# Performance work log

Hardware: AMD Instinct MI355X
Metric: run time of the kernel (lower is better)

## Reference

```python
import jax, jax.numpy as jnp
import numpy as np
import math

B, L, C_IN = 32, 1024, 21
D_MODEL, N_HEADS, D_FF, E_LAYERS = 256, 8, 1024, 3
E = D_MODEL // N_HEADS
MOVING_AVG, FACTOR, NUM_CLASS = 5, 1.0, 3


def setup_inputs() -> dict:
    key = jax.random.key(0)
    ks = jax.random.split(key, 12)
    s = 0.05
    return {
        "x_enc": jax.random.normal(ks[0], (B, L, C_IN), jnp.float32),
        "token_w": jax.random.normal(ks[1], (D_MODEL, C_IN, 3), jnp.float32) * s,
        "qw": jax.random.normal(ks[2], (E_LAYERS, D_MODEL, D_MODEL), jnp.float32) * s,
        "qb": jnp.zeros((E_LAYERS, D_MODEL), jnp.float32),
        "kw": jax.random.normal(ks[3], (E_LAYERS, D_MODEL, D_MODEL), jnp.float32) * s,
        "kb": jnp.zeros((E_LAYERS, D_MODEL), jnp.float32),
        "vw": jax.random.normal(ks[4], (E_LAYERS, D_MODEL, D_MODEL), jnp.float32) * s,
        "vb": jnp.zeros((E_LAYERS, D_MODEL), jnp.float32),
        "ow": jax.random.normal(ks[5], (E_LAYERS, D_MODEL, D_MODEL), jnp.float32) * s,
        "ob": jnp.zeros((E_LAYERS, D_MODEL), jnp.float32),
        "c1w": jax.random.normal(ks[6], (E_LAYERS, D_FF, D_MODEL), jnp.float32) * s,
        "c2w": jax.random.normal(ks[7], (E_LAYERS, D_MODEL, D_FF), jnp.float32) * s,
        "norm_w": jnp.ones((D_MODEL,), jnp.float32),
        "norm_b": jnp.zeros((D_MODEL,), jnp.float32),
        "proj_w": jax.random.normal(ks[8], (NUM_CLASS, D_MODEL * L), jnp.float32) * 0.01,
        "proj_b": jnp.zeros((NUM_CLASS,), jnp.float32),
    }


def moving_mean(x, k):
    # x: (B, L, D); replicate-pad front/end by (k-1)//2 then average (AvgPool1d stride 1)
    p = (k - 1) // 2
    xp = jnp.concatenate([jnp.repeat(x[:, :1], p, 1), x, jnp.repeat(x[:, -1:], p, 1)], axis=1)
    Lx = x.shape[1]
    acc = xp[:, :Lx]
    for i in range(1, k):
        acc = acc + xp[:, i:i + Lx]
    return acc / k


def series_decomp(x, k):
    m = moving_mean(x, k)
    return x - m, m


def autocorrelation(q, k_, v):
    # q,k_,v: (B, L, H, E). Period-based dependency via FFT cross-correlation.
    Lq = q.shape[1]
    qf = jnp.fft.rfft(q.transpose(0, 2, 3, 1), axis=-1)   # (B,H,E,L//2+1)
    kf = jnp.fft.rfft(k_.transpose(0, 2, 3, 1), axis=-1)
    corr = jnp.fft.irfft(qf * jnp.conj(kf), n=Lq, axis=-1)  # (B,H,E,L)
    vals = v.transpose(0, 2, 3, 1)                          # (B,H,E,L)
    top_k = int(FACTOR * math.log(Lq))
    mean_corr = corr.mean(axis=(1, 2))                      # (B,L)
    weights, delay = jax.lax.top_k(mean_corr, top_k)        # (B,k)
    w = jax.nn.softmax(weights, axis=-1)                    # (B,k)
    # rolled gather: pattern[b,h,e,i,l] = vals[b,h,e,(l+delay[b,i]) % L]
    idx = (jnp.arange(Lq)[None, None, :] + delay[:, :, None]) % Lq  # (B,k,L)
    patterns = jax.vmap(lambda vb, ib: vb[:, :, ib])(vals, idx)      # (B,H,E,k,L)
    out = jnp.einsum('bhekl,bk->bhel', patterns, w)
    return out.transpose(0, 3, 1, 2)  # (B,L,H,E)


def encoder_layer(x, qw, qb, kw, kb, vw, vb, ow, ob, c1w, c2w):
    Bx, Lx, _ = x.shape
    q = (x @ qw.T + qb).reshape(Bx, Lx, N_HEADS, E)
    k_ = (x @ kw.T + kb).reshape(Bx, Lx, N_HEADS, E)
    v = (x @ vw.T + vb).reshape(Bx, Lx, N_HEADS, E)
    a = autocorrelation(q, k_, v).reshape(Bx, Lx, D_MODEL)
    a = a @ ow.T + ob
    x, _ = series_decomp(x + a, MOVING_AVG)
    y = jax.nn.gelu(jnp.einsum('bld,fd->blf', x, c1w), approximate=False)  # Conv1d k=1
    y = jnp.einsum('blf,df->bld', y, c2w)
    res, _ = series_decomp(x + y, MOVING_AVG)
    return res


def my_layernorm(x, w, b):
    mu = x.mean(-1, keepdims=True)
    var = ((x - mu) ** 2).mean(-1, keepdims=True)
    xh = (x - mu) / jnp.sqrt(var + 1e-5) * w + b
    return xh - xh.mean(axis=1, keepdims=True)  # subtract seasonal bias over time


def token_embed(x, w):
    # circular-padded Conv1d(C_IN -> D_MODEL, kernel 3, no bias)
    xt = x.transpose(0, 2, 1)                                   # (B,C,L)
    xp = jnp.pad(xt, ((0, 0), (0, 0), (1, 1)), mode='wrap')
    out = jax.lax.conv_general_dilated(xp, w, (1,), 'VALID')     # (B,D,L)
    return out.transpose(0, 2, 1)


def reference(x_enc, token_w, qw, qb, kw, kb, vw, vb, ow, ob, c1w, c2w, norm_w, norm_b, proj_w, proj_b):
    x = token_embed(x_enc, token_w)
    for l in range(E_LAYERS):
        x = encoder_layer(x, qw[l], qb[l], kw[l], kb[l], vw[l], vb[l], ow[l], ob[l], c1w[l], c2w[l])
    x = my_layernorm(x, norm_w, norm_b)
    out = jax.nn.gelu(x, approximate=False)
    out = out.reshape(out.shape[0], -1)  # (B, L*D_MODEL)
    return out @ proj_w.T + proj_b
```

## Files before the change

kernel.cpp:

```cpp
#include <hip/hip_runtime.h>
#include <hip/hip_bf16.h>
#include <math.h>

#define BB 32
#define LL 1024
#define C_IN 21
#define DM 256
#define DFF 1024
#define NLAYERS 3
#define TOPK 6
#define TOPC 16
#define LSCALE 4096.0f
#define LINV (1.0f/4096.0f)

typedef __attribute__((ext_vector_type(8))) short short8v;
typedef __attribute__((ext_vector_type(8))) _Float16 half8;
typedef __attribute__((ext_vector_type(4))) float f32x4;

__device__ __forceinline__ float gelu_f(float v){
    return 0.5f * v * (1.0f + erff(v * 0.7071067811865476f));
}
__device__ __forceinline__ ushort f2h_bits(float f){
    _Float16 h = (_Float16)f;
    return __builtin_bit_cast(ushort, h);
}
__device__ __forceinline__ float h2f(ushort u){
    return (float)__builtin_bit_cast(_Float16, u);
}
__device__ __forceinline__ void lds16(const ushort* g, ushort* l){
    __builtin_amdgcn_global_load_lds(
        (const __attribute__((address_space(1))) void*)g,
        (__attribute__((address_space(3))) void*)l, 16, 0, 0);
}
__device__ __forceinline__ float4 loadp4(const ushort* __restrict__ h, const ushort* __restrict__ l, size_t i4){
    ushort4 hv = *reinterpret_cast<const ushort4*>(h + 4*i4);
    ushort4 lv = *reinterpret_cast<const ushort4*>(l + 4*i4);
    return make_float4(h2f(hv.x)+h2f(lv.x)*LINV, h2f(hv.y)+h2f(lv.y)*LINV,
                       h2f(hv.z)+h2f(lv.z)*LINV, h2f(hv.w)+h2f(lv.w)*LINV);
}
__device__ __forceinline__ void storep4(ushort* __restrict__ h, ushort* __restrict__ l, size_t i4, float4 v){
    ushort4 hv, lv;
    _Float16 a;
    a=(_Float16)v.x; hv.x=__builtin_bit_cast(ushort,a); lv.x=f2h_bits((v.x-(float)a)*LSCALE);
    a=(_Float16)v.y; hv.y=__builtin_bit_cast(ushort,a); lv.y=f2h_bits((v.y-(float)a)*LSCALE);
    a=(_Float16)v.z; hv.z=__builtin_bit_cast(ushort,a); lv.z=f2h_bits((v.z-(float)a)*LSCALE);
    a=(_Float16)v.w; hv.w=__builtin_bit_cast(ushort,a); lv.w=f2h_bits((v.w-(float)a)*LSCALE);
    *reinterpret_cast<ushort4*>(h + 4*i4) = hv;
    *reinterpret_cast<ushort4*>(l + 4*i4) = lv;
}

__global__ __launch_bounds__(256) void split_w_k(const float* __restrict__ src,
                                                 ushort* __restrict__ h, ushort* __restrict__ l, int n){
    int i = blockIdx.x*256 + threadIdx.x;
    if (i < n){
        float f = src[i];
        _Float16 hh = (_Float16)f;
        h[i] = __builtin_bit_cast(ushort, hh);
        l[i] = f2h_bits((f - (float)hh) * LSCALE);
    }
}
__global__ __launch_bounds__(256) void split_w_strided(const float* __restrict__ src,
                                                       ushort* __restrict__ h, ushort* __restrict__ l,
                                                       int n, int src_ls, int dst_ls, int dst_off){
    int i = blockIdx.x*256 + threadIdx.x;
    if (i < n){
        int layer = i / src_ls, r = i % src_ls;
        float f = src[i];
        _Float16 hh = (_Float16)f;
        size_t d = (size_t)layer*dst_ls + dst_off + r;
        h[d] = __builtin_bit_cast(ushort, hh);
        l[d] = f2h_bits((f - (float)hh) * LSCALE);
    }
}
__global__ __launch_bounds__(256) void cat_bias3_k(const float* __restrict__ b1,
                                                   const float* __restrict__ b2,
                                                   const float* __restrict__ b3,
                                                   float* __restrict__ out, int n){
    int i = blockIdx.x*256 + threadIdx.x;
    if (i < n){
        int layer = i / 768, c = i % 768;
        out[i] = (c < 256) ? b1[layer*256 + c]
               : (c < 512) ? b2[layer*256 + c - 256]
                           : b3[layer*256 + c - 512];
    }
}
__global__ __launch_bounds__(256) void transpose_tw(const float* __restrict__ src,
                                                    float* __restrict__ dst){
    int i = blockIdx.x*256 + threadIdx.x;
    if (i < 256*63){
        int d = i / 63, k = i % 63;
        dst[k*256 + d] = src[i];
    }
}

__global__ __launch_bounds__(256) void token_embed_k(const float* __restrict__ x,
                                                     const float* __restrict__ wT,
                                                     ushort* __restrict__ oh,
                                                     ushort* __restrict__ ol){
    int b = blockIdx.x, l0 = blockIdx.y*32;
    int d = threadIdx.x;
    __shared__ float xs[34][C_IN];
    for (int i = threadIdx.x; i < 34*C_IN; i += 256){
        int r = i / C_IN, c = i % C_IN;
        int g = (l0 - 1 + r + LL) & (LL-1);
        xs[r][c] = x[(size_t)b*LL*C_IN + (size_t)g*C_IN + c];
    }
    float w[63];
    #pragma unroll
    for (int k=0;k<63;k++) w[k] = wT[k*256 + d];
    __syncthreads();
    for (int i=0;i<32;i++){
        float acc = 0.f;
        #pragma unroll
        for (int c=0;c<C_IN;c++){
            acc += xs[i][c]   * w[c*3+0];
            acc += xs[i+1][c] * w[c*3+1];
            acc += xs[i+2][c] * w[c*3+2];
        }
        size_t idx = ((size_t)b*LL + l0+i)*DM + d;
        _Float16 hh = (_Float16)acc;
        oh[idx] = __builtin_bit_cast(ushort, hh);
        ol[idx] = f2h_bits((acc - (float)hh) * LSCALE);
    }
}

template<bool BIAS, bool GELU, int OMODE, bool ZSPLIT>
__global__ __launch_bounds__(256) void gemm_mfma_split(const ushort* __restrict__ Ah_g,
                                                       const ushort* __restrict__ Al_g,
                                                       const ushort* __restrict__ Wh,
                                                       const ushort* __restrict__ Wl,
                                                       const float* __restrict__ bias,
                                                       void* __restrict__ Cv,
                                                       void* __restrict__ C2v,
                                                       void* __restrict__ C3v,
                                                       void* __restrict__ C4v,
                                                       void* __restrict__ C5v,
                                                       int M, int N, int K){
    __shared__ __align__(16) ushort Ah_s[2][128*32];
    __shared__ __align__(16) ushort Al_s[2][128*32];
    __shared__ __align__(16) ushort Wh_s[2][64*32];
    __shared__ __align__(16) ushort Wl_s[2][64*32];

    const int tid = threadIdx.x;
    const int MB = M >> 7;
    const int bx = blockIdx.x % MB, by = blockIdx.x / MB;
    const int bm = bx << 7, bn = by << 6;

    const int lane = tid & 63;
    const int wid  = tid >> 6;
    const int wm = wid >> 1, wn = wid & 1;
    const int lr = lane & 15, lg = lane >> 4;

    int aoff[4], boff[2];
    #pragma unroll
    for (int f=0; f<4; f++){
        int ar = wm*64 + f*16 + lr;
        aoff[f] = ar*32 + (lg ^ ((ar>>1)&3))*8;
    }
    #pragma unroll
    for (int g=0; g<2; g++){
        int br = wn*32 + g*16 + lr;
        boff[g] = br*32 + (lg ^ ((br>>1)&3))*8;
    }

    f32x4 acc[4][2], accX[4][2];
    #pragma unroll
    for (int i=0;i<4;i++)
        #pragma unroll
        for (int j=0;j<2;j++){
            acc[i][j]  = (f32x4){0.f,0.f,0.f,0.f};
            accX[i][j] = (f32x4){0.f,0.f,0.f,0.f};
        }

    const int kbeg = ZSPLIT ? (int)blockIdx.y * (K>>1) : 0;
    const int kend = ZSPLIT ? kbeg + (K>>1) : K;
    const int wbase = (tid & 192);

    auto stage = [&](int bufi, int k0){
        #pragma unroll
        for (int i=0;i<2;i++){
            int c = i*256 + tid;
            int row = c >> 2, ko = c & 3;
            int sw = ko ^ ((row>>1)&3);
            size_t src = (size_t)(bm+row)*K + k0 + sw*8;
            int ldso = (i*256 + wbase)*8;
            lds16(Ah_g + src, &Ah_s[bufi][ldso]);
            lds16(Al_g + src, &Al_s[bufi][ldso]);
        }
        {
            int row = tid >> 2, ko = tid & 3;
            int sw = ko ^ ((row>>1)&3);
            size_t src = (size_t)(bn+row)*K + k0 + sw*8;
            lds16(Wh + src, &Wh_s[bufi][wbase*8]);
            lds16(Wl + src, &Wl_s[bufi][wbase*8]);
        }
    };

    stage(0, kbeg);
    __syncthreads();

    int cur = 0;
    for (int k0=kbeg; k0<kend; k0+=32){
        if (k0 + 32 < kend) stage(cur^1, k0+32);

        short8v af[4], al[4], bf_[2], bl[2];
        #pragma unroll
        for (int f=0; f<4; f++){
            af[f] = *reinterpret_cast<short8v*>(&Ah_s[cur][aoff[f]]);
            al[f] = *reinterpret_cast<short8v*>(&Al_s[cur][aoff[f]]);
        }
        #pragma unroll
        for (int g=0; g<2; g++){
            bf_[g] = *reinterpret_cast<short8v*>(&Wh_s[cur][boff[g]]);
            bl[g]  = *reinterpret_cast<short8v*>(&Wl_s[cur][boff[g]]);
        }
        #pragma unroll
        for (int i=0;i<4;i++){
            #pragma unroll
            for (int j=0;j<2;j++){
                acc[i][j] = __builtin_amdgcn_mfma_f32_16x16x32_f16(
                    __builtin_bit_cast(half8, af[i]), __builtin_bit_cast(half8, bf_[j]), acc[i][j], 0,0,0);
                accX[i][j] = __builtin_amdgcn_mfma_f32_16x16x32_f16(
                    __builtin_bit_cast(half8, af[i]), __builtin_bit_cast(half8, bl[j]), accX[i][j], 0,0,0);
                accX[i][j] = __builtin_amdgcn_mfma_f32_16x16x32_f16(
                    __builtin_bit_cast(half8, al[i]), __builtin_bit_cast(half8, bf_[j]), accX[i][j], 0,0,0);
            }
        }
        __syncthreads();
        cur ^= 1;
    }

    float* Cout0 = (float*)((ZSPLIT && blockIdx.y) ? C2v : Cv);
    const int crow0 = bm + wm*64, ccol0 = bn + wn*32;
    #pragma unroll
    for (int i=0;i<4;i++){
        #pragma unroll
        for (int j=0;j<2;j++){
            int row0 = crow0 + i*16 + lg*4;
            int col  = ccol0 + j*16 + lr;
            float bv = (BIAS && (!ZSPLIT || blockIdx.y==0)) ? bias[col] : 0.f;
            #pragma unroll
            for (int r=0;r<4;r++){
                float v = acc[i][j][r] + accX[i][j][r]*LINV + bv;
                if (GELU) v = gelu_f(v);
                if (OMODE == 0){
                    Cout0[(size_t)(row0+r)*N + col] = v;
                } else if (OMODE == 2){
                    size_t idx = (size_t)(row0+r)*N + col;
                    _Float16 hh = (_Float16)v;
                    ((ushort*)Cv)[idx]  = __builtin_bit_cast(ushort, hh);
                    ((ushort*)C2v)[idx] = f2h_bits((v - (float)hh) * LSCALE);
                } else {
                    if (col < 512){
                        _Float16 hh = (_Float16)v;
                        ushort hb = __builtin_bit_cast(ushort, hh);
                        ushort lb = f2h_bits((v - (float)hh) * LSCALE);
                        if (col < 256){
                            size_t idx = (size_t)(row0+r)*256 + col;
                            ((ushort*)Cv)[idx]  = hb;
                            ((ushort*)C2v)[idx] = lb;
                        } else {
                            size_t idx = (size_t)(row0+r)*256 + (col-256);
                            ((ushort*)C3v)[idx] = hb;
                            ((ushort*)C4v)[idx] = lb;
                        }
                    } else {
                        ((float*)C5v)[(size_t)(row0+r)*256 + (col-512)] = v;
                    }
                }
            }
        }
    }
}

__global__ __launch_bounds__(256) void corr_mfma(const ushort* __restrict__ qh,
                                                 const ushort* __restrict__ kh,
                                                 float* __restrict__ scr){
    __shared__ __align__(16) ushort Qh_s[2][128*32];
    __shared__ __align__(16) ushort Kh_s[2][128*32];
    __shared__ float bins[255];

    const int tid = threadIdx.x;
    int flat = blockIdx.x;
    flat = (flat & 7) * 256 + (flat >> 3);
    const int bxt = flat & 7;
    const int byt = (flat >> 3) & 7;
    const int b   = flat >> 6;
    const int bi = bxt * 128, bj = byt * 128;

    for (int i=tid; i<255; i+=256) bins[i] = 0.f;

    const int lane = tid & 63;
    const int wid  = tid >> 6;
    const int wm = wid >> 1, wn = wid & 1;
    const int lr = lane & 15, lg = lane >> 4;

    int aoff[4], boff[4];
    #pragma unroll
    for (int f=0; f<4; f++){
        int ar = wm*64 + f*16 + lr;
        aoff[f] = ar*32 + (lg ^ ((ar>>1)&3))*8;
        int br = wn*64 + f*16 + lr;
        boff[f] = br*32 + (lg ^ ((br>>1)&3))*8;
    }

    f32x4 acc[4][4];
    #pragma unroll
    for (int i=0;i<4;i++)
        #pragma unroll
        for (int j=0;j<4;j++)
            acc[i][j] = (f32x4){0.f,0.f,0.f,0.f};

    const size_t qbase = (size_t)b*LL*DM;
    const int wbase = (tid & 192);

    auto stage = [&](int bufi, int k0){
        #pragma unroll
        for (int i=0;i<2;i++){
            int c = i*256 + tid;
            int row = c >> 2, ko = c & 3;
            int sw = ko ^ ((row>>1)&3);
            size_t qsrc = qbase + (size_t)(bi+row)*DM + k0 + sw*8;
            size_t ksrc = qbase + (size_t)(bj+row)*DM + k0 + sw*8;
            int ldso = (i*256 + wbase)*8;
            lds16(qh + qsrc, &Qh_s[bufi][ldso]);
            lds16(kh + ksrc, &Kh_s[bufi][ldso]);
        }
    };

    stage(0, 0);
    __syncthreads();

    int cur = 0;
    for (int k0=0; k0<DM; k0+=32){
        if (k0 + 32 < DM) stage(cur^1, k0+32);

        short8v ah[4], bh4[4];
        #pragma unroll
        for (int f=0; f<4; f++){
            ah[f]  = *reinterpret_cast<short8v*>(&Qh_s[cur][aoff[f]]);
            bh4[f] = *reinterpret_cast<short8v*>(&Kh_s[cur][boff[f]]);
        }
        #pragma unroll
        for (int i=0;i<4;i++)
            #pragma unroll
            for (int j=0;j<4;j++)
                acc[i][j] = __builtin_amdgcn_mfma_f32_16x16x32_f16(
                    __builtin_bit_cast(half8, ah[i]), __builtin_bit_cast(half8, bh4[j]), acc[i][j], 0,0,0);
        __syncthreads();
        cur ^= 1;
    }

    float pre[7][4];
    #pragma unroll
    for (int d=0; d<7; d++)
        #pragma unroll
        for (int r=0;r<4;r++) pre[d][r]=0.f;
    #pragma unroll
    for (int i=0;i<4;i++)
        #pragma unroll
        for (int j=0;j<4;j++)
            #pragma unroll
            for (int r=0;r<4;r++)
                pre[i-j+3][r] += acc[i][j][r];
    const int bbase = wm*64 - wn*64 + lg*4 - lr + 127;
    #pragma unroll
    for (int d=0; d<7; d++)
        #pragma unroll
        for (int r=0;r<4;r++)
            atomicAdd(&bins[bbase + 16*(d-3) + r], pre[d][r]);
    __syncthreads();
    float* slot = scr + ((size_t)(b*64 + byt*8 + bxt) << 8);
    for (int i=tid; i<255; i+=256) slot[i] = bins[i];
}

__global__ __launch_bounds__(256) void corr_sel(const float* __restrict__ scr,
                                                int* __restrict__ cand){
    int b = blockIdx.x, tid = threadIdx.x;
    __shared__ float sv[LL];
    __shared__ float rv[256];
    __shared__ int ri[256];
    const float* base = scr + ((size_t)b << 14);
    for (int t = tid; t < LL; t += 256){
        float s = 0.f;
        #pragma unroll
        for (int byt=0; byt<8; byt++){
            #pragma unroll
            for (int bxt=0; bxt<8; bxt++){
                int i = (t - 128*(bxt - byt) + 127) & (LL-1);
                if (i < 255) s += base[((byt*8 + bxt) << 8) + i];
            }
        }
        sv[t] = s * (1.f/256.f);
    }
    __syncthreads();
    for (int it=0; it<TOPC; it++){
        float best = -1e30f; int bi = LL;
        for (int i=tid;i<LL;i+=256){
            float v = sv[i];
            if (v > best || (v == best && i < bi)){ best = v; bi = i; }
        }
        rv[tid]=best; ri[tid]=bi;
        __syncthreads();
        for (int s=128;s>0;s>>=1){
            if (tid < s){
                if (rv[tid+s] > rv[tid] || (rv[tid+s]==rv[tid] && ri[tid+s]<ri[tid])){
                    rv[tid]=rv[tid+s]; ri[tid]=ri[tid+s];
                }
            }
            __syncthreads();
        }
        if (tid==0){ cand[b*TOPC+it]=ri[0]; sv[ri[0]] = -1e30f; }
        __syncthreads();
    }
}

__global__ __launch_bounds__(256) void rescore_k(const ushort* __restrict__ qh,
                                                 const ushort* __restrict__ ql,
                                                 const ushort* __restrict__ kh,
                                                 const ushort* __restrict__ kl,
                                                 const int* __restrict__ cand,
                                                 float* __restrict__ scores4){
    int i = blockIdx.x;
    int b = (i & 7) | (((i >> 3) & 3) << 3);
    int c = i >> 5;
    int chunk = blockIdx.y;
    int t = cand[b*TOPC + c];
    const size_t base = (size_t)b << 18;
    const int off = t << 8;
    const int mbeg = chunk << 16;
    const int mend = mbeg + (1<<16);
    float s = 0.f, comp = 0.f;
    for (int m = mbeg + threadIdx.x*8; m < mend; m += 256*8){
        int mq = (m + off) & ((1<<18)-1);
        short8v kh8 = *reinterpret_cast<const short8v*>(kh + base + m);
        short8v kl8 = *reinterpret_cast<const short8v*>(kl + base + m);
        short8v qh8 = *reinterpret_cast<const short8v*>(qh + base + mq);
        short8v ql8 = *reinterpret_cast<const short8v*>(ql + base + mq);
        float term = 0.f;
        #pragma unroll
        for (int j=0;j<8;j++){
            float kf = h2f((ushort)kh8[j]) + h2f((ushort)kl8[j])*LINV;
            float qf = h2f((ushort)qh8[j]) + h2f((ushort)ql8[j])*LINV;
            term += kf*qf;
        }
        float y = term - comp;
        float tt = s + y;
        comp = (tt - s) - y;
        s = tt;
    }
    for (int o=32;o>0;o>>=1) s += __shfl_down(s, o, 64);
    __shared__ float red[4];
    if ((threadIdx.x & 63)==0) red[threadIdx.x>>6] = s;
    __syncthreads();
    if (threadIdx.x==0)
        scores4[(size_t)(b*TOPC + c)*4 + chunk] = red[0]+red[1]+red[2]+red[3];
}

__global__ __launch_bounds__(64) void finalize_k(const int* __restrict__ cand,
                                                 const float* __restrict__ scores4,
                                                 int* __restrict__ delays,
                                                 float* __restrict__ wts){
    int b = blockIdx.x;
    int lane = threadIdx.x;
    float v = -1e30f;
    int idx = 1<<30;
    if (lane < TOPC){
        size_t s4 = (size_t)(b*TOPC + lane)*4;
        v = (scores4[s4] + scores4[s4+1] + scores4[s4+2] + scores4[s4+3]) * (1.f/256.f);
        idx = cand[b*TOPC + lane];
    }
    float topv[TOPK]; int topi[TOPK];
    #pragma unroll
    for (int k=0;k<TOPK;k++){
        float bv = v; int bi = idx;
        #pragma unroll
        for (int o=8;o>0;o>>=1){
            float ov = __shfl_xor(bv, o, 16);
            int   oi = __shfl_xor(bi, o, 16);
            if (ov > bv || (ov == bv && oi < bi)){ bv = ov; bi = oi; }
        }
        topv[k]=bv; topi[k]=bi;
        if (idx == bi) v = -1e30f;
    }
    if (lane==0){
        float mx = topv[0];
        float e[TOPK], se=0.f;
        #pragma unroll
        for (int k=0;k<TOPK;k++){ e[k]=expf(topv[k]-mx); se+=e[k]; }
        #pragma unroll
        for (int k=0;k<TOPK;k++){
            wts[b*TOPK+k] = e[k]/se;
            delays[b*TOPK+k] = topi[k];
        }
    }
}

__global__ __launch_bounds__(256) void attn_gather4(const float4* __restrict__ v,
                                                    const int* __restrict__ delays,
                                                    const float* __restrict__ wts,
                                                    ushort* __restrict__ ah,
                                                    ushort* __restrict__ al){
    int gid = blockIdx.x*256 + threadIdx.x;
    int d4 = gid & 63;
    int bl = gid >> 6;
    int b = bl >> 10, l = bl & (LL-1);
    const int* dl = delays + b*TOPK;
    const float* w = wts + b*TOPK;
    float ax=0.f, ay=0.f, az=0.f, aw=0.f;
    #pragma unroll
    for (int kk=0;kk<TOPK;kk++){
        int ls = (l + dl[kk]) & (LL-1);
        float4 t = v[(size_t)((b<<10)+ls)*64 + d4];
        float wk = w[kk];
        ax += wk*t.x; ay += wk*t.y; az += wk*t.z; aw += wk*t.w;
    }
    storep4(ah, al, gid, make_float4(ax, ay, az, aw));
}

__global__ __launch_bounds__(256) void add_decomp_pf_p(const ushort* __restrict__ xah,
                                                       const ushort* __restrict__ xal,
                                                       const float4* __restrict__ xb,
                                                       ushort* __restrict__ oh,
                                                       ushort* __restrict__ ol){
    int d4 = threadIdx.x & 63;
    int rg = threadIdx.x >> 6;
    int b = blockIdx.x;
    int l0 = blockIdx.y*128 + rg*32;
    float4 win[5];
    #pragma unroll
    for (int i=0;i<4;i++){
        int g = l0 - 2 + i;
        g = g < 0 ? 0 : g;
        size_t idx = (size_t)((b<<10) + g)*64 + d4;
        float4 A = loadp4(xah, xal, idx), Bv = xb[idx];
        win[i] = make_float4(A.x+Bv.x, A.y+Bv.y, A.z+Bv.z, A.w+Bv.w);
    }
    for (int i=0;i<32;i++){
        int g = l0 + 2 + i;
        g = g > LL-1 ? LL-1 : g;
        size_t idx = (size_t)((b<<10) + g)*64 + d4;
        float4 A = loadp4(xah, xal, idx), Bv = xb[idx];
        win[4] = make_float4(A.x+Bv.x, A.y+Bv.y, A.z+Bv.z, A.w+Bv.w);
        float4 o;
        o.x = win[2].x - (win[0].x+win[1].x+win[2].x+win[3].x+win[4].x)*0.2f;
        o.y = win[2].y - (win[0].y+win[1].y+win[2].y+win[3].y+win[4].y)*0.2f;
        o.z = win[2].z - (win[0].z+win[1].z+win[2].z+win[3].z+win[4].z)*0.2f;
        o.w = win[2].w - (win[0].w+win[1].w+win[2].w+win[3].w+win[4].w)*0.2f;
        storep4(oh, ol, (size_t)((b<<10) + l0 + i)*64 + d4, o);
        win[0]=win[1]; win[1]=win[2]; win[2]=win[3]; win[3]=win[4];
    }
}

__global__ __launch_bounds__(256) void add_decomp3_pff_p(const ushort* __restrict__ xah,
                                                         const ushort* __restrict__ xal,
                                                         const float4* __restrict__ xb,
                                                         const float4* __restrict__ xc,
                                                         ushort* __restrict__ oh,
                                                         ushort* __restrict__ ol){
    int d4 = threadIdx.x & 63;
    int rg = threadIdx.x >> 6;
    int b = blockIdx.x;
    int l0 = blockIdx.y*128 + rg*32;
    float4 win[5];
    #pragma unroll
    for (int i=0;i<4;i++){
        int g = l0 - 2 + i;
        g = g < 0 ? 0 : g;
        size_t idx = (size_t)((b<<10) + g)*64 + d4;
        float4 A = loadp4(xah, xal, idx), Bv = xb[idx], Cc = xc[idx];
        win[i] = make_float4(A.x+Bv.x+Cc.x, A.y+Bv.y+Cc.y, A.z+Bv.z+Cc.z, A.w+Bv.w+Cc.w);
    }
    for (int i=0;i<32;i++){
        int g = l0 + 2 + i;
        g = g > LL-1 ? LL-1 : g;
        size_t idx = (size_t)((b<<10) + g)*64 + d4;
        float4 A = loadp4(xah, xal, idx), Bv = xb[idx], Cc = xc[idx];
        win[4] = make_float4(A.x+Bv.x+Cc.x, A.y+Bv.y+Cc.y, A.z+Bv.z+Cc.z, A.w+Bv.w+Cc.w);
        float4 o;
        o.x = win[2].x - (win[0].x+win[1].x+win[2].x+win[3].x+win[4].x)*0.2f;
        o.y = win[2].y - (win[0].y+win[1].y+win[2].y+win[3].y+win[4].y)*0.2f;
        o.z = win[2].z - (win[0].z+win[1].z+win[2].z+win[3].z+win[4].z)*0.2f;
        o.w = win[2].w - (win[0].w+win[1].w+win[2].w+win[3].w+win[4].w)*0.2f;
        storep4(oh, ol, (size_t)((b<<10) + l0 + i)*64 + d4, o);
        win[0]=win[1]; win[1]=win[2]; win[2]=win[3]; win[3]=win[4];
    }
}

__global__ __launch_bounds__(256) void ln_kernel(const ushort* __restrict__ xh_,
                                                 const ushort* __restrict__ xl_,
                                                 const float* __restrict__ nw,
                                                 const float* __restrict__ nb,
                                                 float* __restrict__ xh){
    int bl = blockIdx.x, d = threadIdx.x;
    size_t i = (size_t)bl*DM + d;
    float val = h2f(xh_[i]) + h2f(xl_[i])*LINV;
    __shared__ float red[4];
    float v = val;
    for (int o=32;o>0;o>>=1) v += __shfl_down(v, o, 64);
    if ((d&63)==0) red[d>>6] = v;
    __syncthreads();
    float mu = (red[0]+red[1]+red[2]+red[3])*(1.f/256.f);
    __syncthreads();
    float diff = val - mu;
    v = diff*diff;
    for (int o=32;o>0;o>>=1) v += __shfl_down(v, o, 64);
    if ((d&63)==0) red[d>>6] = v;
    __syncthreads();
    float var = (red[0]+red[1]+red[2]+red[3])*(1.f/256.f);
    xh[i] = diff*rsqrtf(var+1e-5f)*nw[d] + nb[d];
}

__global__ __launch_bounds__(256) void colsum_kernel(const float* __restrict__ xh,
                                                     float* __restrict__ colsum){
    int b = blockIdx.x, chunk = blockIdx.y, d = threadIdx.x;
    float s = 0.f;
    for (int l = chunk*128; l < (chunk+1)*128; l++)
        s += xh[((size_t)b*LL + l)*DM + d];
    atomicAdd(&colsum[b*DM + d], s);
}

__global__ __launch_bounds__(256) void gelu_sub_kernel(const float* __restrict__ xh,
                                                       const float* __restrict__ colsum,
                                                       float* __restrict__ g){
    int bl = blockIdx.x, d = threadIdx.x;
    int b = bl / LL;
    float v = xh[(size_t)bl*DM + d] - colsum[b*DM + d]*(1.f/1024.f);
    g[(size_t)bl*DM + d] = gelu_f(v);
}

__global__ __launch_bounds__(256) void proj_kernel(const float* __restrict__ g,
                                                   const float* __restrict__ pw,
                                                   const float* __restrict__ pb,
                                                   float* __restrict__ out){
    int b = blockIdx.x, c = blockIdx.y, ch = blockIdx.z;
    int tid = threadIdx.x;
    const size_t F = (size_t)LL*DM;
    size_t base = ch*(F/16);
    float s = 0.f;
    for (size_t i = tid; i < F/16; i += 256)
        s += g[(size_t)b*F + base + i] * pw[(size_t)c*F + base + i];
    for (int o=32;o>0;o>>=1) s += __shfl_down(s, o, 64);
    __shared__ float red[4];
    if ((tid&63)==0) red[tid>>6] = s;
    __syncthreads();
    if (tid==0){
        float tot = red[0]+red[1]+red[2]+red[3];
        if (ch==0) tot += pb[c];
        atomicAdd(&out[b*3 + c], tot);
    }
}

extern "C" void kernel_launch(void* const* d_in, const int* in_sizes, int n_in,
                              void* d_out, int out_size, void* d_ws, size_t ws_size,
                              hipStream_t stream) {
    const float* x_enc   = (const float*)d_in[0];
    const float* token_w = (const float*)d_in[1];
    const float* qw = (const float*)d_in[2];
    const float* qb = (const float*)d_in[3];
    const float* kw = (const float*)d_in[4];
    const float* kb = (const float*)d_in[5];
    const float* vw = (const float*)d_in[6];
    const float* vb = (const float*)d_in[7];
    const float* ow = (const float*)d_in[8];
    const float* ob = (const float*)d_in[9];
    const float* c1w = (const float*)d_in[10];
    const float* c2w = (const float*)d_in[11];
    const float* norm_w = (const float*)d_in[12];
    const float* norm_b = (const float*)d_in[13];
    const float* proj_w = (const float*)d_in[14];
    const float* proj_b = (const float*)d_in[15];
    float* outp = (float*)d_out;

    const size_t NTOK = (size_t)BB*LL*DM;
    float* ws = (float*)d_ws;
    float* buf0 = ws;
    float* buf1 = ws + NTOK;
    float* buf2 = ws + 2*NTOK;
    ushort* wu = (ushort*)(ws + 3*NTOK);
    const size_t WSM = (size_t)NLAYERS*DM*DM;
    const size_t WSF = (size_t)NLAYERS*DFF*DM;
    ushort* qkvwh = wu;              ushort* qkvwl = qkvwh + 3*WSM;
    ushort* owh  = qkvwl + 3*WSM;    ushort* owl  = owh + WSM;
    ushort* c1wh = owl + WSM;        ushort* c1wl = c1wh + WSF;
    ushort* c2wh = c1wl + WSF;       ushort* c2wl = c2wh + WSF;
    float* after_w = ws + 3*NTOK + 2359296;
    float* qkvbias = after_w;
    float* colsum = qkvbias + (size_t)NLAYERS*768;
    int*   delays = (int*)(colsum + BB*DM);
    float* wts    = (float*)(delays + BB*TOPK);
    int*   cand   = (int*)(wts + BB*TOPK);
    float* scores4 = (float*)(cand + BB*TOPC);
    float* twT    = scores4 + BB*TOPC*4;
    float* scr    = twT + 63*256;
    float* buf3   = scr + 524288;

    const size_t needed_floats = 3*NTOK + 2359296 + (size_t)NLAYERS*768 + (size_t)BB*DM
                               + (size_t)BB*TOPK*2 + (size_t)BB*TOPC
                               + (size_t)BB*TOPC*4 + 63*256 + 524288 + NTOK;
    const bool zs = (ws_size >= needed_floats*sizeof(float));

    hipMemsetAsync(d_out, 0, 96*sizeof(float), stream);

    {
        int n1 = NLAYERS*DM*DM;
        int n2 = NLAYERS*DFF*DM;
        split_w_strided<<<(n1+255)/256, 256, 0, stream>>>(qw, qkvwh, qkvwl, n1, 65536, 196608, 0);
        split_w_strided<<<(n1+255)/256, 256, 0, stream>>>(kw, qkvwh, qkvwl, n1, 65536, 196608, 65536);
        split_w_strided<<<(n1+255)/256, 256, 0, stream>>>(vw, qkvwh, qkvwl, n1, 65536, 196608, 131072);
        cat_bias3_k<<<(NLAYERS*768+255)/256, 256, 0, stream>>>(qb, kb, vb, qkvbias, NLAYERS*768);
        split_w_k<<<(n1+255)/256, 256, 0, stream>>>(ow, owh, owl, n1);
        split_w_k<<<(n2+255)/256, 256, 0, stream>>>(c1w, c1wh, c1wl, n2);
        split_w_k<<<(n2+255)/256, 256, 0, stream>>>(c2w, c2wh, c2wl, n2);
        transpose_tw<<<(256*63+255)/256, 256, 0, stream>>>(token_w, twT);
    }

    ushort* xh_p = (ushort*)buf0;  ushort* xl_p = xh_p + NTOK;
    token_embed_k<<<dim3(BB, LL/32), 256, 0, stream>>>(x_enc, twT, xh_p, xl_p);

    const int M = BB*LL;
    const int FFNC = 8192;

    for (int l=0; l<NLAYERS; l++){
        ushort* qkvwh_l = qkvwh + (size_t)l*768*DM; ushort* qkvwl_l = qkvwl + (size_t)l*768*DM;
        ushort* owh_l = owh + (size_t)l*DM*DM;      ushort* owl_l = owl + (size_t)l*DM*DM;
        ushort* c1wh_l = c1wh + (size_t)l*DFF*DM;   ushort* c1wl_l = c1wl + (size_t)l*DFF*DM;
        ushort* c2wh_l = c2wh + (size_t)l*DM*DFF;   ushort* c2wl_l = c2wl + (size_t)l*DM*DFF;
        const float* qkvb_l = qkvbias + (size_t)l*768;
        const float* ob_l = ob + (size_t)l*DM;

        ushort* qh_p = (ushort*)buf1;  ushort* ql_p = qh_p + NTOK;
        ushort* kh_p = (ushort*)buf2;  ushort* kl_p = kh_p + NTOK;
        gemm_mfma_split<true,false,4,false><<<(M/128)*(768/64), 256, 0, stream>>>(
            xh_p, xl_p, qkvwh_l, qkvwl_l, qkvb_l, qh_p, ql_p, kh_p, kl_p, buf3, M, 768, DM);

        corr_mfma<<<2048, 256, 0, stream>>>(qh_p, kh_p, scr);
        corr_sel<<<BB, 256, 0, stream>>>(scr, cand);
        rescore_k<<<dim3(BB*TOPC, 4), 256, 0, stream>>>(qh_p, ql_p, kh_p, kl_p, cand, scores4);
        finalize_k<<<BB, 64, 0, stream>>>(cand, scores4, delays, wts);

        ushort* ah_p = (ushort*)buf1;  ushort* al_p = ah_p + NTOK;
        attn_gather4<<<(BB*LL*64)/256, 256, 0, stream>>>(
            (const float4*)buf3, delays, wts, ah_p, al_p);
        gemm_mfma_split<true,false,0,false><<<(M/128)*(DM/64), 256, 0, stream>>>(
            ah_p, al_p, owh_l, owl_l, ob_l, buf2, nullptr, nullptr, nullptr, nullptr, M, DM, DM);

        ushort* x1h_p = (ushort*)buf1;  ushort* x1l_p = x1h_p + NTOK;
        add_decomp_pf_p<<<dim3(BB, LL/128), 256, 0, stream>>>(
            xh_p, xl_p, (const float4*)buf2, x1h_p, x1l_p);

        ushort* yh_p = (ushort*)buf0;
        ushort* yl_p = yh_p + (size_t)FFNC*DFF;
        for (int c0 = 0; c0 < M; c0 += FFNC){
            gemm_mfma_split<false,true,2,false><<<(FFNC/128)*(DFF/64), 256, 0, stream>>>(
                x1h_p + (size_t)c0*DM, x1l_p + (size_t)c0*DM, c1wh_l, c1wl_l, nullptr,
                yh_p, yl_p, nullptr, nullptr, nullptr, FFNC, DFF, DM);
            if (zs){
                gemm_mfma_split<false,false,0,true><<<dim3((FFNC/128)*(DM/64), 2), 256, 0, stream>>>(
                    yh_p, yl_p, c2wh_l, c2wl_l, nullptr,
                    buf2 + (size_t)c0*DM, buf3 + (size_t)c0*DM, nullptr, nullptr, nullptr, FFNC, DM, DFF);
            } else {
                gemm_mfma_split<false,false,0,false><<<(FFNC/128)*(DM/64), 256, 0, stream>>>(
                    yh_p, yl_p, c2wh_l, c2wl_l, nullptr,
                    buf2 + (size_t)c0*DM, nullptr, nullptr, nullptr, nullptr, FFNC, DM, DFF);
            }
        }

        if (zs)
            add_decomp3_pff_p<<<dim3(BB, LL/128), 256, 0, stream>>>(
                x1h_p, x1l_p, (const float4*)buf2, (const float4*)buf3, xh_p, xl_p);
        else
            add_decomp_pf_p<<<dim3(BB, LL/128), 256, 0, stream>>>(
                x1h_p, x1l_p, (const float4*)buf2, xh_p, xl_p);
    }

    ln_kernel<<<BB*LL, 256, 0, stream>>>(xh_p, xl_p, norm_w, norm_b, buf1);
    hipMemsetAsync(colsum, 0, (size_t)BB*DM*sizeof(float), stream);
    colsum_kernel<<<dim3(BB, 8), 256, 0, stream>>>(buf1, colsum);
    gelu_sub_kernel<<<BB*LL, 256, 0, stream>>>(buf1, colsum, buf2);
    proj_kernel<<<dim3(BB, 3, 16), 256, 0, stream>>>(buf2, proj_w, proj_b, outp);
}
```

Before: 1.782 ms.

## Share K loads across candidates in rescore and drop split-K FFN path

The rescore kernel now has one block per batch and K-chunk, evaluating all 16 candidate delays per loaded K vector instead of one block per candidate. This reuses the K data and cuts K reads, but it adds register pressure, a serialized 16-pass reduction, and fewer blocks (512 instead of 2048). The split-K second FFN GEMM and its three-input decomposition kernel are removed, and the FFN chunk size doubles, with the low half stored in buf3 to halve the chunk loop launches. This lowers launch count and extra partial-sum traffic, but the c2 GEMM now has less grid parallelism per launch.

```diff
diff --git a/kernel.cpp b/kernel.cpp
--- a/kernel.cpp
+++ b/kernel.cpp
@@ -124,7 +124,7 @@
     }
 }
 
-template<bool BIAS, bool GELU, int OMODE, bool ZSPLIT>
+template<bool BIAS, bool GELU, int OMODE>
 __global__ __launch_bounds__(256) void gemm_mfma_split(const ushort* __restrict__ Ah_g,
                                                        const ushort* __restrict__ Al_g,
                                                        const ushort* __restrict__ Wh,
@@ -172,8 +172,6 @@
             accX[i][j] = (f32x4){0.f,0.f,0.f,0.f};
         }
 
-    const int kbeg = ZSPLIT ? (int)blockIdx.y * (K>>1) : 0;
-    const int kend = ZSPLIT ? kbeg + (K>>1) : K;
     const int wbase = (tid & 192);
 
     auto stage = [&](int bufi, int k0){
@@ -196,12 +194,12 @@
         }
     };
 
-    stage(0, kbeg);
+    stage(0, 0);
     __syncthreads();
 
     int cur = 0;
-    for (int k0=kbeg; k0<kend; k0+=32){
-        if (k0 + 32 < kend) stage(cur^1, k0+32);
+    for (int k0=0; k0<K; k0+=32){
+        if (k0 + 32 < K) stage(cur^1, k0+32);
 
         short8v af[4], al[4], bf_[2], bl[2];
         #pragma unroll
@@ -230,7 +228,6 @@
         cur ^= 1;
     }
 
-    float* Cout0 = (float*)((ZSPLIT && blockIdx.y) ? C2v : Cv);
     const int crow0 = bm + wm*64, ccol0 = bn + wn*32;
     #pragma unroll
     for (int i=0;i<4;i++){
@@ -238,13 +235,13 @@
         for (int j=0;j<2;j++){
             int row0 = crow0 + i*16 + lg*4;
             int col  = ccol0 + j*16 + lr;
-            float bv = (BIAS && (!ZSPLIT || blockIdx.y==0)) ? bias[col] : 0.f;
+            float bv = BIAS ? bias[col] : 0.f;
             #pragma unroll
             for (int r=0;r<4;r++){
                 float v = acc[i][j][r] + accX[i][j][r]*LINV + bv;
                 if (GELU) v = gelu_f(v);
                 if (OMODE == 0){
-                    Cout0[(size_t)(row0+r)*N + col] = v;
+                    ((float*)Cv)[(size_t)(row0+r)*N + col] = v;
                 } else if (OMODE == 2){
                     size_t idx = (size_t)(row0+r)*N + col;
                     _Float16 hh = (_Float16)v;
@@ -420,45 +417,55 @@
                                                  const ushort* __restrict__ kh,
                                                  const ushort* __restrict__ kl,
                                                  const int* __restrict__ cand,
-                                                 float* __restrict__ scores4){
-    int i = blockIdx.x;
-    int b = (i & 7) | (((i >> 3) & 3) << 3);
-    int c = i >> 5;
+                                                 float* __restrict__ scores16){
+    int b = blockIdx.x;
     int chunk = blockIdx.y;
-    int t = cand[b*TOPC + c];
+    __shared__ int offs[TOPC];
+    if (threadIdx.x < TOPC) offs[threadIdx.x] = cand[b*TOPC + threadIdx.x] << 8;
+    __syncthreads();
     const size_t base = (size_t)b << 18;
-    const int off = t << 8;
-    const int mbeg = chunk << 16;
-    const int mend = mbeg + (1<<16);
-    float s = 0.f, comp = 0.f;
+    const int mbeg = chunk << 14;
+    const int mend = mbeg + (1<<14);
+    float s[TOPC], comp[TOPC];
+    #pragma unroll
+    for (int c=0;c<TOPC;c++){ s[c]=0.f; comp[c]=0.f; }
     for (int m = mbeg + threadIdx.x*8; m < mend; m += 256*8){
-        int mq = (m + off) & ((1<<18)-1);
         short8v kh8 = *reinterpret_cast<const short8v*>(kh + base + m);
         short8v kl8 = *reinterpret_cast<const short8v*>(kl + base + m);
-        short8v qh8 = *reinterpret_cast<const short8v*>(qh + base + mq);
-        short8v ql8 = *reinterpret_cast<const short8v*>(ql + base + mq);
-        float term = 0.f;
-        #pragma unroll
-        for (int j=0;j<8;j++){
-            float kf = h2f((ushort)kh8[j]) + h2f((ushort)kl8[j])*LINV;
-            float qf = h2f((ushort)qh8[j]) + h2f((ushort)ql8[j])*LINV;
-            term += kf*qf;
-        }
-        float y = term - comp;
-        float tt = s + y;
-        comp = (tt - s) - y;
-        s = tt;
-    }
-    for (int o=32;o>0;o>>=1) s += __shfl_down(s, o, 64);
+        float kf[8];
+        #pragma unroll
+        for (int j=0;j<8;j++)
+            kf[j] = h2f((ushort)kh8[j]) + h2f((ushort)kl8[j])*LINV;
+        #pragma unroll
+        for (int c=0;c<TOPC;c++){
+            int mq = (m + offs[c]) & ((1<<18)-1);
+            short8v qh8 = *reinterpret_cast<const short8v*>(qh + base + mq);
+            short8v ql8 = *reinterpret_cast<const short8v*>(ql + base + mq);
+            float term = 0.f;
+            #pragma unroll
+            for (int j=0;j<8;j++)
+                term += kf[j] * (h2f((ushort)qh8[j]) + h2f((ushort)ql8[j])*LINV);
+            float y = term - comp[c];
+            float tt = s[c] + y;
+            comp[c] = (tt - s[c]) - y;
+            s[c] = tt;
+        }
+    }
     __shared__ float red[4];
-    if ((threadIdx.x & 63)==0) red[threadIdx.x>>6] = s;
-    __syncthreads();
-    if (threadIdx.x==0)
-        scores4[(size_t)(b*TOPC + c)*4 + chunk] = red[0]+red[1]+red[2]+red[3];
+    #pragma unroll
+    for (int c=0;c<TOPC;c++){
+        float v = s[c];
+        for (int o=32;o>0;o>>=1) v += __shfl_down(v, o, 64);
+        if ((threadIdx.x & 63)==0) red[threadIdx.x>>6] = v;
+        __syncthreads();
+        if (threadIdx.x==0)
+            scores16[((size_t)b*TOPC + c)*16 + chunk] = red[0]+red[1]+red[2]+red[3];
+        __syncthreads();
+    }
 }
 
 __global__ __launch_bounds__(64) void finalize_k(const int* __restrict__ cand,
-                                                 const float* __restrict__ scores4,
+                                                 const float* __restrict__ scores16,
                                                  int* __restrict__ delays,
                                                  float* __restrict__ wts){
     int b = blockIdx.x;
@@ -466,8 +473,11 @@
     float v = -1e30f;
     int idx = 1<<30;
     if (lane < TOPC){
-        size_t s4 = (size_t)(b*TOPC + lane)*4;
-        v = (scores4[s4] + scores4[s4+1] + scores4[s4+2] + scores4[s4+3]) * (1.f/256.f);
+        size_t s16 = ((size_t)b*TOPC + lane)*16;
+        float acc = 0.f;
+        #pragma unroll
+        for (int ch=0; ch<16; ch++) acc += scores16[s16+ch];
+        v = acc * (1.f/256.f);
         idx = cand[b*TOPC + lane];
     }
     float topv[TOPK]; int topi[TOPK];
@@ -542,41 +552,6 @@
         size_t idx = (size_t)((b<<10) + g)*64 + d4;
         float4 A = loadp4(xah, xal, idx), Bv = xb[idx];
         win[4] = make_float4(A.x+Bv.x, A.y+Bv.y, A.z+Bv.z, A.w+Bv.w);
-        float4 o;
-        o.x = win[2].x - (win[0].x+win[1].x+win[2].x+win[3].x+win[4].x)*0.2f;
-        o.y = win[2].y - (win[0].y+win[1].y+win[2].y+win[3].y+win[4].y)*0.2f;
-        o.z = win[2].z - (win[0].z+win[1].z+win[2].z+win[3].z+win[4].z)*0.2f;
-        o.w = win[2].w - (win[0].w+win[1].w+win[2].w+win[3].w+win[4].w)*0.2f;
-        storep4(oh, ol, (size_t)((b<<10) + l0 + i)*64 + d4, o);
-        win[0]=win[1]; win[1]=win[2]; win[2]=win[3]; win[3]=win[4];
-    }
-}
-
-__global__ __launch_bounds__(256) void add_decomp3_pff_p(const ushort* __restrict__ xah,
-                                                         const ushort* __restrict__ xal,
-                                                         const float4* __restrict__ xb,
-                                                         const float4* __restrict__ xc,
-                                                         ushort* __restrict__ oh,
-                                                         ushort* __restrict__ ol){
-    int d4 = threadIdx.x & 63;
-    int rg = threadIdx.x >> 6;
-    int b = blockIdx.x;
-    int l0 = blockIdx.y*128 + rg*32;
-    float4 win[5];
-    #pragma unroll
-    for (int i=0;i<4;i++){
-        int g = l0 - 2 + i;
-        g = g < 0 ? 0 : g;
-        size_t idx = (size_t)((b<<10) + g)*64 + d4;
-        float4 A = loadp4(xah, xal, idx), Bv = xb[idx], Cc = xc[idx];
-        win[i] = make_float4(A.x+Bv.x+Cc.x, A.y+Bv.y+Cc.y, A.z+Bv.z+Cc.z, A.w+Bv.w+Cc.w);
-    }
-    for (int i=0;i<32;i++){
-        int g = l0 + 2 + i;
-        g = g > LL-1 ? LL-1 : g;
-        size_t idx = (size_t)((b<<10) + g)*64 + d4;
-        float4 A = loadp4(xah, xal, idx), Bv = xb[idx], Cc = xc[idx];
-        win[4] = make_float4(A.x+Bv.x+Cc.x, A.y+Bv.y+Cc.y, A.z+Bv.z+Cc.z, A.w+Bv.w+Cc.w);
         float4 o;
         o.x = win[2].x - (win[0].x+win[1].x+win[2].x+win[3].x+win[4].x)*0.2f;
         o.y = win[2].y - (win[0].y+win[1].y+win[2].y+win[3].y+win[4].y)*0.2f;
@@ -690,15 +665,10 @@
     int*   delays = (int*)(colsum + BB*DM);
     float* wts    = (float*)(delays + BB*TOPK);
     int*   cand   = (int*)(wts + BB*TOPK);
-    float* scores4 = (float*)(cand + BB*TOPC);
-    float* twT    = scores4 + BB*TOPC*4;
+    float* scores16 = (float*)(cand + BB*TOPC);
+    float* twT    = scores16 + BB*TOPC*16;
     float* scr    = twT + 63*256;
     float* buf3   = scr + 524288;
-
-    const size_t needed_floats = 3*NTOK + 2359296 + (size_t)NLAYERS*768 + (size_t)BB*DM
-                               + (size_t)BB*TOPK*2 + (size_t)BB*TOPC
-                               + (size_t)BB*TOPC*4 + 63*256 + 524288 + NTOK;
-    const bool zs = (ws_size >= needed_floats*sizeof(float));
 
     hipMemsetAsync(d_out, 0, 96*sizeof(float), stream);
 
@@ -719,7 +689,7 @@
     token_embed_k<<<dim3(BB, LL/32), 256, 0, stream>>>(x_enc, twT, xh_p, xl_p);
 
     const int M = BB*LL;
-    const int FFNC = 8192;
+    const int FFNC = 16384;
 
     for (int l=0; l<NLAYERS; l++){
         ushort* qkvwh_l = qkvwh + (size_t)l*768*DM; ushort* qkvwl_l = qkvwl + (size_t)l*768*DM;
@@ -731,18 +701,18 @@
 
         ushort* qh_p = (ushort*)buf1;  ushort* ql_p = qh_p + NTOK;
         ushort* kh_p = (ushort*)buf2;  ushort* kl_p = kh_p + NTOK;
-        gemm_mfma_split<true,false,4,false><<<(M/128)*(768/64), 256, 0, stream>>>(
+        gemm_mfma_split<true,false,4><<<(M/128)*(768/64), 256, 0, stream>>>(
             xh_p, xl_p, qkvwh_l, qkvwl_l, qkvb_l, qh_p, ql_p, kh_p, kl_p, buf3, M, 768, DM);
 
         corr_mfma<<<2048, 256, 0, stream>>>(qh_p, kh_p, scr);
         corr_sel<<<BB, 256, 0, stream>>>(scr, cand);
-        rescore_k<<<dim3(BB*TOPC, 4), 256, 0, stream>>>(qh_p, ql_p, kh_p, kl_p, cand, scores4);
-        finalize_k<<<BB, 64, 0, stream>>>(cand, scores4, delays, wts);
+        rescore_k<<<dim3(BB, 16), 256, 0, stream>>>(qh_p, ql_p, kh_p, kl_p, cand, scores16);
+        finalize_k<<<BB, 64, 0, stream>>>(cand, scores16, delays, wts);
 
         ushort* ah_p = (ushort*)buf1;  ushort* al_p = ah_p + NTOK;
         attn_gather4<<<(BB*LL*64)/256, 256, 0, stream>>>(
             (const float4*)buf3, delays, wts, ah_p, al_p);
-        gemm_mfma_split<true,false,0,false><<<(M/128)*(DM/64), 256, 0, stream>>>(
+        gemm_mfma_split<true,false,0><<<(M/128)*(DM/64), 256, 0, stream>>>(
             ah_p, al_p, owh_l, owl_l, ob_l, buf2, nullptr, nullptr, nullptr, nullptr, M, DM, DM);
 
         ushort* x1h_p = (ushort*)buf1;  ushort* x1l_p = x1h_p + NTOK;
@@ -750,28 +720,18 @@
             xh_p, xl_p, (const float4*)buf2, x1h_p, x1l_p);
 
         ushort* yh_p = (ushort*)buf0;
-        ushort* yl_p = yh_p + (size_t)FFNC*DFF;
+        ushort* yl_p = (ushort*)buf3;
         for (int c0 = 0; c0 < M; c0 += FFNC){
-            gemm_mfma_split<false,true,2,false><<<(FFNC/128)*(DFF/64), 256, 0, stream>>>(
+            gemm_mfma_split<false,true,2><<<(FFNC/128)*(DFF/64), 256, 0, stream>>>(
                 x1h_p + (size_t)c0*DM, x1l_p + (size_t)c0*DM, c1wh_l, c1wl_l, nullptr,
                 yh_p, yl_p, nullptr, nullptr, nullptr, FFNC, DFF, DM);
-            if (zs){
-                gemm_mfma_split<false,false,0,true><<<dim3((FFNC/128)*(DM/64), 2), 256, 0, stream>>>(
-                    yh_p, yl_p, c2wh_l, c2wl_l, nullptr,
-                    buf2 + (size_t)c0*DM, buf3 + (size_t)c0*DM, nullptr, nullptr, nullptr, FFNC, DM, DFF);
-            } else {
-                gemm_mfma_split<false,false,0,false><<<(FFNC/128)*(DM/64), 256, 0, stream>>>(
-                    yh_p, yl_p, c2wh_l, c2wl_l, nullptr,
-                    buf2 + (size_t)c0*DM, nullptr, nullptr, nullptr, nullptr, FFNC, DM, DFF);
-            }
-        }
-
-        if (zs)
-            add_decomp3_pff_p<<<dim3(BB, LL/128), 256, 0, stream>>>(
-                x1h_p, x1l_p, (const float4*)buf2, (const float4*)buf3, xh_p, xl_p);
-        else
-            add_decomp_pf_p<<<dim3(BB, LL/128), 256, 0, stream>>>(
-                x1h_p, x1l_p, (const float4*)buf2, xh_p, xl_p);
+            gemm_mfma_split<false,false,0><<<(FFNC/128)*(DM/64), 256, 0, stream>>>(
+                yh_p, yl_p, c2wh_l, c2wl_l, nullptr,
+                buf2 + (size_t)c0*DM, nullptr, nullptr, nullptr, nullptr, FFNC, DM, DFF);
+        }
+
+        add_decomp_pf_p<<<dim3(BB, LL/128), 256, 0, stream>>>(
+            x1h_p, x1l_p, (const float4*)buf2, xh_p, xl_p);
     }
 
     ln_kernel<<<BB*LL, 256, 0, stream>>>(xh_p, xl_p, norm_w, norm_b, buf1);
```

Measured after the change: 1.658 ms. 1.08x faster.
